# Performance work log

Hardware: AMD Instinct MI355X
Metric: run time of the kernel (lower is better)

Reference implementation:

```python
import jax, jax.numpy as jnp
import numpy as np

N, D, C = 8192, 1024, 1000
T_SCALE = 0.3
LAM2 = 0.1


def setup_inputs() -> dict:
    key = jax.random.key(0)
    k1, k2, k3 = jax.random.split(key, 3)
    feat = jax.random.normal(k1, (N, D), dtype=jnp.float32)
    W = jax.random.normal(k2, (C, D), dtype=jnp.float32) * 0.02
    b = jnp.zeros((C,), dtype=jnp.float32)
    labels = jax.random.randint(k3, (N,), 0, C)
    return {"feat": feat, "labels": labels, "W": W, "b": b}


def _scl_loss(feat_n, labels, t):
    # feat_n: l2-normalized features [N, D]
    n = feat_n.shape[0]
    sim = (feat_n @ feat_n.T) / t                      # [N, N]
    eye = jnp.eye(n, dtype=bool)
    # denominator: sum_{k != i} exp(sim[i,k])  (log-domain, same math)
    bottom_log = jax.nn.logsumexp(jnp.where(eye, -jnp.inf, sim), axis=1)  # [N]
    # positive mask: same label, j != i
    pos = (labels[:, None] == labels[None, :]) & ~eye  # [N, N]
    counts = pos.sum(axis=1)                           # [N]
    # log(exp(sim_ij)/bottom_i) = sim_ij - bottom_log_i
    sum_log = jnp.sum(jnp.where(pos, sim - bottom_log[:, None], 0.0), axis=1)
    valid = counts > 0
    per_sample = jnp.where(valid, -sum_log / jnp.maximum(counts, 1), 0.0)
    n_valid = valid.sum()
    return jnp.where(n_valid > 0, per_sample.sum() / jnp.maximum(n_valid, 1), 0.0)


def reference(feat, labels, W, b):
    logits = feat @ W.T + b                            # [N, C]
    # cross entropy (mean over batch)
    logp = jax.nn.log_softmax(logits, axis=-1)
    ce = -jnp.mean(jnp.take_along_axis(logp, labels[:, None], axis=1)[:, 0])
    # supervised contrastive loss on l2-normalized features
    feat_n = feat / jnp.linalg.norm(feat, axis=1, keepdims=True)
    scl = _scl_loss(feat_n, labels, T_SCALE)
    loss = (1.0 - LAM2) * ce + LAM2 * scl
    return logits, loss
```

## Files before the change

kernel.cpp:

```cpp
#include <hip/hip_runtime.h>
#include <hip/hip_bf16.h>
#include <math.h>

#define N 8192
#define D 1024
#define C 1000
#define CP 1024
#define INV_T (1.0f / 0.3f)

typedef __bf16 bf16_t;
typedef bf16_t bf16x8 __attribute__((ext_vector_type(8)));
typedef float f32x4 __attribute__((ext_vector_type(4)));

typedef __attribute__((address_space(3))) uint32_t lds_u32_t;
typedef const __attribute__((address_space(1))) uint32_t glb_u32_t;

__global__ void prep_kernel(const float* __restrict__ feat, const int* __restrict__ labels,
                            const float* __restrict__ W,
                            float* __restrict__ norms, bf16_t* __restrict__ feat_n,
                            bf16_t* __restrict__ Wp, int* __restrict__ hist) {
  int g = blockIdx.x;
  int t = threadIdx.x;
  if (g < N) {
    int row = g;
    const float4* fr = (const float4*)(feat + (size_t)row * D);
    float4 x = fr[t];
    float ss = x.x * x.x + x.y * x.y + x.z * x.z + x.w * x.w;
    for (int off = 32; off; off >>= 1) ss += __shfl_down(ss, off, 64);
    __shared__ float sred[4];
    __shared__ float srn;
    int lane = t & 63, w = t >> 6;
    if (lane == 0) sred[w] = ss;
    __syncthreads();
    if (t == 0) {
      float tot = sred[0] + sred[1] + sred[2] + sred[3];
      float nrm = sqrtf(tot);
      norms[row] = nrm;
      srn = 1.0f / nrm;
      atomicAdd(&hist[labels[row]], 1);
    }
    __syncthreads();
    float rn = srn;
    union { bf16_t h[4]; uint2 u; } pk;
    pk.h[0] = (bf16_t)(x.x * rn);
    pk.h[1] = (bf16_t)(x.y * rn);
    pk.h[2] = (bf16_t)(x.z * rn);
    pk.h[3] = (bf16_t)(x.w * rn);
    *(uint2*)(feat_n + (size_t)row * D + t * 4) = pk.u;
  } else {
    int row = g - N;
    union { bf16_t h[4]; uint2 u; } pk;
    if (row < C) {
      float4 x = ((const float4*)(W + (size_t)row * D))[t];
      pk.h[0] = (bf16_t)x.x; pk.h[1] = (bf16_t)x.y;
      pk.h[2] = (bf16_t)x.z; pk.h[3] = (bf16_t)x.w;
    } else {
      pk.h[0] = pk.h[1] = pk.h[2] = pk.h[3] = (bf16_t)0.0f;
    }
    *(uint2*)(Wp + (size_t)row * D + t * 4) = pk.u;
  }
}

#define BM 128
#define BN 128
#define BK 64
#define NSIM 2080

__device__ __forceinline__ void stage_tile(const bf16_t* __restrict__ g0,
                                           bf16_t* lds, int t, int w) {
#pragma unroll
  for (int p = 0; p < 4; p++) {
    int chunk = p * 256 + t;
    int r = chunk >> 3;
    int c = (chunk & 7) ^ (r & 7);
    const bf16_t* gp = g0 + (size_t)r * D + c * 8;
    bf16_t* lp = lds + (size_t)(p * 256 + w * 64) * 8;
    __builtin_amdgcn_global_load_lds((glb_u32_t*)gp, (lds_u32_t*)lp, 16, 0, 0);
  }
}

__launch_bounds__(256)
__global__ void logits_gemm(const bf16_t* __restrict__ A, const bf16_t* __restrict__ Wp,
                            const float* __restrict__ norms, const float* __restrict__ bias,
                            float* __restrict__ ceS, float* __restrict__ out) {
  __shared__ __align__(16) bf16_t As[BM * BK];
  __shared__ __align__(16) bf16_t Bs[BN * BK];
  int tileM = blockIdx.x * BM;
  int tileN = blockIdx.y * BN;
  int t = threadIdx.x;
  int lane = t & 63;
  int w = t >> 6;
  int wm = (w & 1) << 6;
  int wn = (w >> 1) << 6;
  int l15 = lane & 15;
  int quad = lane >> 4;
  f32x4 acc[4][4] = {};
  const bf16_t* Abase = A + (size_t)tileM * D;
  const bf16_t* Bbase = Wp + (size_t)tileN * D;

  for (int k0 = 0; k0 < D; k0 += BK) {
    stage_tile(Abase + k0, As, t, w);
    stage_tile(Bbase + k0, Bs, t, w);
    __syncthreads();
#pragma unroll
    for (int h = 0; h < 2; h++) {
      bf16x8 af[4], bfr[4];
#pragma unroll
      for (int i = 0; i < 4; i++) {
        int ar = wm + i * 16 + l15;
        int cc = (h * 4 + quad) ^ (ar & 7);
        af[i] = *(const bf16x8*)(&As[ar * BK + cc * 8]);
      }
#pragma unroll
      for (int j = 0; j < 4; j++) {
        int br = wn + j * 16 + l15;
        int cc = (h * 4 + quad) ^ (br & 7);
        bfr[j] = *(const bf16x8*)(&Bs[br * BK + cc * 8]);
      }
#pragma unroll
      for (int i = 0; i < 4; i++)
#pragma unroll
        for (int j = 0; j < 4; j++)
          acc[i][j] = __builtin_amdgcn_mfma_f32_16x16x32_bf16(af[i], bfr[j], acc[i][j], 0, 0, 0);
    }
    __syncthreads();
  }
#pragma unroll
  for (int i = 0; i < 4; i++) {
#pragma unroll
    for (int r = 0; r < 4; r++) {
      int gr = tileM + wm + i * 16 + quad * 4 + r;
      float nrm = norms[gr];
      float esum = 0.0f;
#pragma unroll
      for (int j = 0; j < 4; j++) {
        int gc = tileN + wn + j * 16 + l15;
        if (gc < C) {
          float lg = nrm * acc[i][j][r] + bias[gc];
          out[(size_t)gr * C + gc] = lg;
          esum += __expf(lg);
        }
      }
      for (int m = 1; m < 16; m <<= 1) esum += __shfl_xor(esum, m, 64);
      if (l15 == 0) atomicAdd(&ceS[gr], esum);
    }
  }
}

__launch_bounds__(256)
__global__ void sim_gemm(const bf16_t* __restrict__ A, const int* __restrict__ labels,
                         float* __restrict__ S, float* __restrict__ P) {
  __shared__ __align__(16) bf16_t As[BM * BK];
  __shared__ __align__(16) bf16_t Bs[BN * BK];
  int g = blockIdx.x;
  int t = threadIdx.x;
  int lane = t & 63;
  int w = t >> 6;
  int wm = (w & 1) << 6;
  int wn = (w >> 1) << 6;
  int l15 = lane & 15;
  int quad = lane >> 4;
  f32x4 acc[4][4] = {};

  const int nb = N / BM;
  float fnb = (float)nb + 0.5f;
  int bi = (int)(fnb - sqrtf(fnb * fnb - 2.0f * (float)g));
  if (bi < 0) bi = 0;
#define TRI_OFF(r) ((r) * nb - (r) * ((r)-1) / 2)
  while (TRI_OFF(bi + 1) <= g) bi++;
  while (TRI_OFF(bi) > g) bi--;
  int bj = bi + (g - TRI_OFF(bi));
#undef TRI_OFF
  bi = __builtin_amdgcn_readfirstlane(bi);
  bj = __builtin_amdgcn_readfirstlane(bj);
  int tileM = bi * BM;
  int tileN = bj * BN;
  bool diag = (bi == bj);

  const bf16_t* Abase = A + (size_t)tileM * D;
  const bf16_t* Bbase = A + (size_t)tileN * D;

  for (int k0 = 0; k0 < D; k0 += BK) {
    stage_tile(Abase + k0, As, t, w);
    stage_tile(Bbase + k0, Bs, t, w);
    __syncthreads();
#pragma unroll
    for (int h = 0; h < 2; h++) {
      bf16x8 af[4], bfr[4];
#pragma unroll
      for (int i = 0; i < 4; i++) {
        int ar = wm + i * 16 + l15;
        int cc = (h * 4 + quad) ^ (ar & 7);
        af[i] = *(const bf16x8*)(&As[ar * BK + cc * 8]);
      }
#pragma unroll
      for (int j = 0; j < 4; j++) {
        int br = wn + j * 16 + l15;
        int cc = (h * 4 + quad) ^ (br & 7);
        bfr[j] = *(const bf16x8*)(&Bs[br * BK + cc * 8]);
      }
#pragma unroll
      for (int i = 0; i < 4; i++)
#pragma unroll
        for (int j = 0; j < 4; j++)
          acc[i][j] = __builtin_amdgcn_mfma_f32_16x16x32_bf16(af[i], bfr[j], acc[i][j], 0, 0, 0);
    }
    __syncthreads();
  }

  int gcj[4], lc[4];
#pragma unroll
  for (int j = 0; j < 4; j++) {
    gcj[j] = tileN + wn + j * 16 + l15;
    lc[j] = labels[gcj[j]];
  }
  float csS[4] = {0.f, 0.f, 0.f, 0.f}, csP[4] = {0.f, 0.f, 0.f, 0.f};
#pragma unroll
  for (int i = 0; i < 4; i++) {
#pragma unroll
    for (int r = 0; r < 4; r++) {
      int gr = tileM + wm + i * 16 + quad * 4 + r;
      int lr = labels[gr];
      float ssum = 0.0f, psum = 0.0f;
#pragma unroll
      for (int j = 0; j < 4; j++) {
        float sim = acc[i][j][r] * INV_T;
        if (gcj[j] != gr) {
          float e = __expf(sim);
          float pv = (lc[j] == lr) ? sim : 0.0f;
          ssum += e;
          psum += pv;
          csS[j] += e;
          csP[j] += pv;
        }
      }
      for (int m = 1; m < 16; m <<= 1) {
        ssum += __shfl_xor(ssum, m, 64);
        psum += __shfl_xor(psum, m, 64);
      }
      if (l15 == 0) {
        atomicAdd(&S[gr], ssum);
        atomicAdd(&P[gr], psum);
      }
    }
  }
  if (!diag) {
#pragma unroll
    for (int j = 0; j < 4; j++) {
      csS[j] += __shfl_xor(csS[j], 16, 64);
      csS[j] += __shfl_xor(csS[j], 32, 64);
      csP[j] += __shfl_xor(csP[j], 16, 64);
      csP[j] += __shfl_xor(csP[j], 32, 64);
      if (quad == 0) {
        atomicAdd(&S[gcj[j]], csS[j]);
        atomicAdd(&P[gcj[j]], csP[j]);
      }
    }
  }
}

__global__ void final_partial(const float* __restrict__ S, const float* __restrict__ P,
                              const int* __restrict__ labels, const int* __restrict__ hist,
                              const float* __restrict__ ceS, const float* __restrict__ out,
                              float* __restrict__ accums) {
  int i = blockIdx.x * 256 + threadIdx.x;
  int lab = labels[i];
  float cesum = logf(ceS[i]) - out[(size_t)i * C + lab];
  float lsum = 0.0f, lval = 0.0f;
  int cnt = hist[lab] - 1;
  if (cnt > 0) {
    float bl = logf(S[i]);
    lsum = -(P[i] - (float)cnt * bl) / (float)cnt;
    lval = 1.0f;
  }
  for (int off = 32; off; off >>= 1) {
    cesum += __shfl_down(cesum, off, 64);
    lsum += __shfl_down(lsum, off, 64);
    lval += __shfl_down(lval, off, 64);
  }
  __shared__ float sc[4], ss[4], sv[4];
  int lane = threadIdx.x & 63, w = threadIdx.x >> 6;
  if (lane == 0) { sc[w] = cesum; ss[w] = lsum; sv[w] = lval; }
  __syncthreads();
  if (threadIdx.x == 0) {
    atomicAdd(&accums[0], sc[0] + sc[1] + sc[2] + sc[3]);
    atomicAdd(&accums[1], ss[0] + ss[1] + ss[2] + ss[3]);
    atomicAdd(&accums[2], sv[0] + sv[1] + sv[2] + sv[3]);
  }
}

__global__ void loss_kernel(const float* __restrict__ accums, float* __restrict__ out) {
  float ce = accums[0] * (1.0f / (float)N);
  float nv = accums[2];
  float scl = (nv > 0.0f) ? accums[1] / nv : 0.0f;
  out[(size_t)N * C] = 0.9f * ce + 0.1f * scl;
}

extern "C" void kernel_launch(void* const* d_in, const int* in_sizes, int n_in,
                              void* d_out, int out_size, void* d_ws, size_t ws_size,
                              hipStream_t stream) {
  const float* feat   = (const float*)d_in[0];
  const int*   labels = (const int*)d_in[1];
  const float* W      = (const float*)d_in[2];
  const float* b      = (const float*)d_in[3];
  float* out = (float*)d_out;

  char* ws = (char*)d_ws;
  bf16_t* feat_n = (bf16_t*)ws;
  bf16_t* Wp     = (bf16_t*)(ws + (size_t)N * D * 2);
  float*  norms  = (float*)(ws + (size_t)N * D * 2 + (size_t)CP * D * 2);
  float*  S      = norms + N;
  float*  P      = S + N;
  float*  ceS    = P + N;
  int*    hist   = (int*)(ceS + N);
  float*  accums = (float*)(hist + 1024);

  size_t zero_bytes = (size_t)((char*)(accums + 4) - (char*)S);
  hipMemsetAsync(S, 0, zero_bytes, stream);

  prep_kernel<<<N + CP, 256, 0, stream>>>(feat, labels, W, norms, feat_n, Wp, hist);
  logits_gemm<<<dim3(N / BM, CP / BN), 256, 0, stream>>>(feat_n, Wp, norms, b, ceS, out);
  sim_gemm<<<NSIM, 256, 0, stream>>>(feat_n, labels, S, P);
  final_partial<<<N / 256, 256, 0, stream>>>(S, P, labels, hist, ceS, out, accums);
  loss_kernel<<<1, 1, 0, stream>>>(accums, out);
}
```

Before: 266.8 us.

## Use FP8 for similarity GEMM and fold memset and loss kernel into others

Normalized features are also quantized to FP8 (scaled by 16) in the prep kernel, and the N×N similarity GEMM now runs on fp8 MFMA, with the scale undone in the epilogue. This halves operand bytes per K-step and uses the higher-throughput fp8 MFMA path. The memset is replaced by extra zeroing blocks in prep, the label histogram moves to a per-block LDS histogram in the final kernel, and the final loss is computed by the last block through an atomic counter instead of a separate launch. FP8 quantization reduces the accuracy of the similarity values feeding exp and the positive sums, which risks tolerance failures.

```diff
diff --git a/kernel.cpp b/kernel.cpp
--- a/kernel.cpp
+++ b/kernel.cpp
@@ -7,6 +7,7 @@
 #define C 1000
 #define CP 1024
 #define INV_T (1.0f / 0.3f)
+#define SIM_SCALE (INV_T / 256.0f)
 
 typedef __bf16 bf16_t;
 typedef bf16_t bf16x8 __attribute__((ext_vector_type(8)));
@@ -15,10 +16,14 @@
 typedef __attribute__((address_space(3))) uint32_t lds_u32_t;
 typedef const __attribute__((address_space(1))) uint32_t glb_u32_t;
 
-__global__ void prep_kernel(const float* __restrict__ feat, const int* __restrict__ labels,
+#define ZBYTES (3 * N * 4 + 16)
+#define NZB 25
+
+__global__ void prep_kernel(const float* __restrict__ feat,
                             const float* __restrict__ W,
                             float* __restrict__ norms, bf16_t* __restrict__ feat_n,
-                            bf16_t* __restrict__ Wp, int* __restrict__ hist) {
+                            unsigned int* __restrict__ feat_f8,
+                            bf16_t* __restrict__ Wp, char* __restrict__ zbase) {
   int g = blockIdx.x;
   int t = threadIdx.x;
   if (g < N) {
@@ -37,7 +42,6 @@
       float nrm = sqrtf(tot);
       norms[row] = nrm;
       srn = 1.0f / nrm;
-      atomicAdd(&hist[labels[row]], 1);
     }
     __syncthreads();
     float rn = srn;
@@ -47,7 +51,12 @@
     pk.h[2] = (bf16_t)(x.z * rn);
     pk.h[3] = (bf16_t)(x.w * rn);
     *(uint2*)(feat_n + (size_t)row * D + t * 4) = pk.u;
-  } else {
+    float rs = rn * 16.0f;
+    unsigned int u8 = 0;
+    u8 = __builtin_amdgcn_cvt_pk_fp8_f32(x.x * rs, x.y * rs, u8, false);
+    u8 = __builtin_amdgcn_cvt_pk_fp8_f32(x.z * rs, x.w * rs, u8, true);
+    feat_f8[(size_t)row * 256 + t] = u8;
+  } else if (g < N + CP) {
     int row = g - N;
     union { bf16_t h[4]; uint2 u; } pk;
     if (row < C) {
@@ -58,6 +67,12 @@
       pk.h[0] = pk.h[1] = pk.h[2] = pk.h[3] = (bf16_t)0.0f;
     }
     *(uint2*)(Wp + (size_t)row * D + t * 4) = pk.u;
+  } else {
+    size_t off = (size_t)(g - N - CP) * 4096 + (size_t)t * 16;
+    if (off < (size_t)ZBYTES) {
+      int4 z = {0, 0, 0, 0};
+      *(int4*)(zbase + off) = z;
+    }
   }
 }
 
@@ -66,8 +81,8 @@
 #define BK 64
 #define NSIM 2080
 
-__device__ __forceinline__ void stage_tile(const bf16_t* __restrict__ g0,
-                                           bf16_t* lds, int t, int w) {
+__device__ __forceinline__ void stage_tile_bf16(const bf16_t* __restrict__ g0,
+                                                bf16_t* lds, int t, int w) {
 #pragma unroll
   for (int p = 0; p < 4; p++) {
     int chunk = p * 256 + t;
@@ -75,6 +90,19 @@
     int c = (chunk & 7) ^ (r & 7);
     const bf16_t* gp = g0 + (size_t)r * D + c * 8;
     bf16_t* lp = lds + (size_t)(p * 256 + w * 64) * 8;
+    __builtin_amdgcn_global_load_lds((glb_u32_t*)gp, (lds_u32_t*)lp, 16, 0, 0);
+  }
+}
+
+__device__ __forceinline__ void stage_tile_f8(const unsigned char* __restrict__ g0,
+                                              unsigned char* lds, int t, int w) {
+#pragma unroll
+  for (int p = 0; p < 2; p++) {
+    int chunk = p * 256 + t;
+    int r = chunk >> 2;
+    int c = (chunk & 3) ^ ((r >> 1) & 3);
+    const unsigned char* gp = g0 + (size_t)r * D + c * 16;
+    unsigned char* lp = lds + (size_t)(p * 256 + w * 64) * 16;
     __builtin_amdgcn_global_load_lds((glb_u32_t*)gp, (lds_u32_t*)lp, 16, 0, 0);
   }
 }
@@ -99,8 +127,8 @@
   const bf16_t* Bbase = Wp + (size_t)tileN * D;
 
   for (int k0 = 0; k0 < D; k0 += BK) {
-    stage_tile(Abase + k0, As, t, w);
-    stage_tile(Bbase + k0, Bs, t, w);
+    stage_tile_bf16(Abase + k0, As, t, w);
+    stage_tile_bf16(Bbase + k0, Bs, t, w);
     __syncthreads();
 #pragma unroll
     for (int h = 0; h < 2; h++) {
@@ -148,10 +176,10 @@
 }
 
 __launch_bounds__(256)
-__global__ void sim_gemm(const bf16_t* __restrict__ A, const int* __restrict__ labels,
+__global__ void sim_gemm(const unsigned char* __restrict__ A8, const int* __restrict__ labels,
                          float* __restrict__ S, float* __restrict__ P) {
-  __shared__ __align__(16) bf16_t As[BM * BK];
-  __shared__ __align__(16) bf16_t Bs[BN * BK];
+  __shared__ __align__(16) unsigned char As[BM * 64];
+  __shared__ __align__(16) unsigned char Bs[BN * 64];
   int g = blockIdx.x;
   int t = threadIdx.x;
   int lane = t & 63;
@@ -177,33 +205,35 @@
   int tileN = bj * BN;
   bool diag = (bi == bj);
 
-  const bf16_t* Abase = A + (size_t)tileM * D;
-  const bf16_t* Bbase = A + (size_t)tileN * D;
+  const unsigned char* Abase = A8 + (size_t)tileM * D;
+  const unsigned char* Bbase = A8 + (size_t)tileN * D;
 
   for (int k0 = 0; k0 < D; k0 += BK) {
-    stage_tile(Abase + k0, As, t, w);
-    stage_tile(Bbase + k0, Bs, t, w);
+    stage_tile_f8(Abase + k0, As, t, w);
+    stage_tile_f8(Bbase + k0, Bs, t, w);
     __syncthreads();
 #pragma unroll
     for (int h = 0; h < 2; h++) {
-      bf16x8 af[4], bfr[4];
+      long af[4], bfr[4];
 #pragma unroll
       for (int i = 0; i < 4; i++) {
         int ar = wm + i * 16 + l15;
-        int cc = (h * 4 + quad) ^ (ar & 7);
-        af[i] = *(const bf16x8*)(&As[ar * BK + cc * 8]);
+        int c8 = h * 4 + quad;
+        int boff = ((c8 >> 1) ^ ((ar >> 1) & 3)) * 16 + (c8 & 1) * 8;
+        af[i] = *(const long*)(&As[ar * 64 + boff]);
       }
 #pragma unroll
       for (int j = 0; j < 4; j++) {
         int br = wn + j * 16 + l15;
-        int cc = (h * 4 + quad) ^ (br & 7);
-        bfr[j] = *(const bf16x8*)(&Bs[br * BK + cc * 8]);
+        int c8 = h * 4 + quad;
+        int boff = ((c8 >> 1) ^ ((br >> 1) & 3)) * 16 + (c8 & 1) * 8;
+        bfr[j] = *(const long*)(&Bs[br * 64 + boff]);
       }
 #pragma unroll
       for (int i = 0; i < 4; i++)
 #pragma unroll
         for (int j = 0; j < 4; j++)
-          acc[i][j] = __builtin_amdgcn_mfma_f32_16x16x32_bf16(af[i], bfr[j], acc[i][j], 0, 0, 0);
+          acc[i][j] = __builtin_amdgcn_mfma_f32_16x16x32_fp8_fp8(af[i], bfr[j], acc[i][j], 0, 0, 0);
     }
     __syncthreads();
   }
@@ -224,7 +254,7 @@
       float ssum = 0.0f, psum = 0.0f;
 #pragma unroll
       for (int j = 0; j < 4; j++) {
-        float sim = acc[i][j][r] * INV_T;
+        float sim = acc[i][j][r] * SIM_SCALE;
         if (gcj[j] != gr) {
           float e = __expf(sim);
           float pv = (lc[j] == lr) ? sim : 0.0f;
@@ -259,15 +289,22 @@
   }
 }
 
-__global__ void final_partial(const float* __restrict__ S, const float* __restrict__ P,
-                              const int* __restrict__ labels, const int* __restrict__ hist,
-                              const float* __restrict__ ceS, const float* __restrict__ out,
-                              float* __restrict__ accums) {
-  int i = blockIdx.x * 256 + threadIdx.x;
+__global__ void final_kernel(const float* __restrict__ S, const float* __restrict__ P,
+                             const int* __restrict__ labels,
+                             const float* __restrict__ ceS, float* __restrict__ out,
+                             float* __restrict__ accums) {
+  __shared__ int lh[1024];
+  int t = threadIdx.x;
+  for (int i = t; i < 1024; i += 256) lh[i] = 0;
+  __syncthreads();
+  for (int i = t; i < N; i += 256) atomicAdd(&lh[labels[i]], 1);
+  __syncthreads();
+
+  int i = blockIdx.x * 256 + t;
   int lab = labels[i];
   float cesum = logf(ceS[i]) - out[(size_t)i * C + lab];
   float lsum = 0.0f, lval = 0.0f;
-  int cnt = hist[lab] - 1;
+  int cnt = lh[lab] - 1;
   if (cnt > 0) {
     float bl = logf(S[i]);
     lsum = -(P[i] - (float)cnt * bl) / (float)cnt;
@@ -279,21 +316,24 @@
     lval += __shfl_down(lval, off, 64);
   }
   __shared__ float sc[4], ss[4], sv[4];
-  int lane = threadIdx.x & 63, w = threadIdx.x >> 6;
+  int lane = t & 63, w = t >> 6;
   if (lane == 0) { sc[w] = cesum; ss[w] = lsum; sv[w] = lval; }
   __syncthreads();
-  if (threadIdx.x == 0) {
+  if (t == 0) {
     atomicAdd(&accums[0], sc[0] + sc[1] + sc[2] + sc[3]);
     atomicAdd(&accums[1], ss[0] + ss[1] + ss[2] + ss[3]);
     atomicAdd(&accums[2], sv[0] + sv[1] + sv[2] + sv[3]);
-  }
-}
-
-__global__ void loss_kernel(const float* __restrict__ accums, float* __restrict__ out) {
-  float ce = accums[0] * (1.0f / (float)N);
-  float nv = accums[2];
-  float scl = (nv > 0.0f) ? accums[1] / nv : 0.0f;
-  out[(size_t)N * C] = 0.9f * ce + 0.1f * scl;
+    __threadfence();
+    unsigned int prev = atomicAdd((unsigned int*)&accums[3], 1u);
+    if (prev == 31) {
+      float a0 = atomicAdd(&accums[0], 0.0f);
+      float a1 = atomicAdd(&accums[1], 0.0f);
+      float a2 = atomicAdd(&accums[2], 0.0f);
+      float ce = a0 * (1.0f / (float)N);
+      float scl = (a2 > 0.0f) ? a1 / a2 : 0.0f;
+      out[(size_t)N * C] = 0.9f * ce + 0.1f * scl;
+    }
+  }
 }
 
 extern "C" void kernel_launch(void* const* d_in, const int* in_sizes, int n_in,
@@ -306,21 +346,18 @@
   float* out = (float*)d_out;
 
   char* ws = (char*)d_ws;
-  bf16_t* feat_n = (bf16_t*)ws;
-  bf16_t* Wp     = (bf16_t*)(ws + (size_t)N * D * 2);
-  float*  norms  = (float*)(ws + (size_t)N * D * 2 + (size_t)CP * D * 2);
+  bf16_t*       feat_n  = (bf16_t*)ws;
+  bf16_t*       Wp      = (bf16_t*)(ws + (size_t)N * D * 2);
+  unsigned int* feat_f8 = (unsigned int*)(ws + (size_t)N * D * 2 + (size_t)CP * D * 2);
+  float*  norms  = (float*)((char*)feat_f8 + (size_t)N * D);
   float*  S      = norms + N;
   float*  P      = S + N;
   float*  ceS    = P + N;
-  int*    hist   = (int*)(ceS + N);
-  float*  accums = (float*)(hist + 1024);
-
-  size_t zero_bytes = (size_t)((char*)(accums + 4) - (char*)S);
-  hipMemsetAsync(S, 0, zero_bytes, stream);
-
-  prep_kernel<<<N + CP, 256, 0, stream>>>(feat, labels, W, norms, feat_n, Wp, hist);
+  float*  accums = ceS + N;
+
+  prep_kernel<<<N + CP + NZB, 256, 0, stream>>>(feat, W, norms, feat_n, feat_f8,
+                                                Wp, (char*)S);
   logits_gemm<<<dim3(N / BM, CP / BN), 256, 0, stream>>>(feat_n, Wp, norms, b, ceS, out);
-  sim_gemm<<<NSIM, 256, 0, stream>>>(feat_n, labels, S, P);
-  final_partial<<<N / 256, 256, 0, stream>>>(S, P, labels, hist, ceS, out, accums);
-  loss_kernel<<<1, 1, 0, stream>>>(accums, out);
-}
+  sim_gemm<<<NSIM, 256, 0, stream>>>((const unsigned char*)feat_f8, labels, S, P);
+  final_kernel<<<N / 256, 256, 0, stream>>>(S, P, labels, ceS, out, accums);
+}
```

New measurement: 248.8 us. 6.7% less time.
